# Kernel optimization log

Measured on AMD Instinct MI355X. Metric: run time of the kernel, lower is better.

Reference implementation:

```python
import jax, jax.numpy as jnp
import numpy as np
import math

B, S, I, C = 1, 512, 512, 256   # batch, n_seqs, n_res, c_in
H, D = 8, 32                    # num_heads, head_dim; total_dim = H*D = 256
TD = H * D


def setup_inputs() -> dict:
    key = jax.random.key(0)
    ks = jax.random.split(key, 12)
    w = lambda k, shape: (jax.random.normal(k, shape, dtype=jnp.float32) * 0.02)
    msa_representation = jax.random.normal(ks[0], (B, S, I, C), dtype=jnp.float32)
    msa_mask = (jax.random.uniform(ks[1], (B, S, I)) > 0.1).astype(jnp.float32)
    return {
        "msa_representation": msa_representation,
        "msa_mask": msa_mask,
        "ln_gamma": jnp.ones((C,), jnp.float32),
        "ln_beta": jnp.zeros((C,), jnp.float32),
        "Wq": w(ks[2], (C, TD)),
        "Wk": w(ks[3], (C, D)),
        "Wv": w(ks[4], (C, D)),
        "Wg": w(ks[5], (C, TD)),
        "bg": jnp.ones((TD,), jnp.float32),   # gate bias init = 1 (init_gate_linear)
        "Wo": w(ks[6], (TD, C)),
        "bo": jnp.zeros((C,), jnp.float32),
    }


def _layer_norm(x, gamma, beta, eps=1e-5):
    mu = jnp.mean(x, axis=-1, keepdims=True)
    var = jnp.mean(jnp.square(x - mu), axis=-1, keepdims=True)
    return (x - mu) * jax.lax.rsqrt(var + eps) * gamma + beta


def reference(msa_representation, msa_mask, ln_gamma, ln_beta,
              Wq, Wk, Wv, Wg, bg, Wo, bo):
    b, s, i, _ = msa_representation.shape
    x_ln = _layer_norm(msa_representation, ln_gamma, ln_beta)

    # Shared (head-less) K, V: [b, s, i, D]
    K = jnp.einsum('bsic,cd->bsid', x_ln, Wk)
    V = jnp.einsum('bsic,cd->bsid', x_ln, Wv)

    # Per-head query: [b, s, i, H, D]
    Q_si = jnp.einsum('bsic,ce->bsie', x_ln, Wq).reshape(b, s, i, H, D)

    # Masked mean-pool of the query over the sequence axis s -> [b, i, H, D]
    qm = msa_mask[..., None, None]                       # [b, s, i, 1, 1]
    Q = (Q_si * qm).sum(axis=1) / jnp.clip(qm.sum(axis=1), 1.0, None)

    # Sigmoid gate: [b, s, i, H, D]
    G = jax.nn.sigmoid(jnp.einsum('bsic,ce->bsie', x_ln, Wg) + bg).reshape(b, s, i, H, D)

    # Scores over the sequence axis t: [b, t, i, H]
    scores = jnp.einsum('bihc,btic->btih', Q, K) / math.sqrt(D)
    scores = scores + (1.0 - msa_mask[:, :, :, None]) * (-1e9)
    attention = jax.nn.softmax(scores, axis=1)

    # Weighted sum of shared V: [b, i, H, D], broadcast over s via gating
    weighted = jnp.einsum('btih,btic->bihc', attention, V)[:, None]  # [b,1,i,H,D]
    gated = (G * weighted).reshape(b, s, i, TD)
    output = jnp.einsum('bsie,ec->bsic', gated, Wo) + bo
    output = output * msa_mask[..., None]
    return output
```

## Files before the change

### kernel.cpp

```cpp
#include <hip/hip_runtime.h>

typedef __bf16 bf16_t;
typedef __bf16 bf16x4 __attribute__((ext_vector_type(4)));
typedef __bf16 bf16x8 __attribute__((ext_vector_type(8)));
typedef float f32x4 __attribute__((ext_vector_type(4)));

#define LXS 264

#define GLOAD_LDS16(gsrc, ldst) \
    __builtin_amdgcn_global_load_lds((__attribute__((address_space(1))) void*)(gsrc), \
                                     (__attribute__((address_space(3))) void*)(ldst), 16, 0, 0)

__global__ __launch_bounds__(256) void k_prep(
    const float* __restrict__ Wg, const float* __restrict__ Wo,
    const float* __restrict__ Wk, const float* __restrict__ Wv,
    bf16_t* __restrict__ WgP, bf16_t* __restrict__ WoP, bf16_t* __restrict__ WKVP)
{
    int id = blockIdx.x * 256 + threadIdx.x;
    if (id < 65536) {
        int j = id & 7, l = (id >> 3) & 63, kt = (id >> 9) & 7, nt = id >> 12;
        int k = kt * 32 + (l >> 4) * 8 + j;
        int n = nt * 16 + (l & 15);
        WgP[id] = (bf16_t)Wg[k * 256 + n];
    } else if (id < 131072) {
        int t = id - 65536;
        int j = t & 7, l = (t >> 3) & 63, kt = (t >> 9) & 7, nt = t >> 12;
        int k = kt * 32 + (l >> 4) * 8 + j;
        int n = nt * 16 + (l & 15);
        WoP[t] = (bf16_t)Wo[k * 256 + n];
    } else if (id < 147456) {
        int t = id - 131072;
        int j = t & 7, l = (t >> 3) & 63, kt = (t >> 9) & 7, nt = t >> 12;
        int k = kt * 32 + (l >> 4) * 8 + j;
        int n = nt * 16 + (l & 15);
        WKVP[t] = (bf16_t)(n < 32 ? Wk[k * 32 + n] : Wv[k * 32 + (n - 32)]);
    }
}

__global__ __launch_bounds__(256) void kA(
    const float* __restrict__ msa, const float* __restrict__ mask,
    const float* __restrict__ gamma, const float* __restrict__ beta,
    bf16_t* __restrict__ xln, bf16_t* __restrict__ kv, const bf16_t* __restrict__ WKVP,
    float* __restrict__ Qpart, float* __restrict__ Qcnt)
{
    __shared__ __align__(16) bf16_t lx[64 * LXS];
    __shared__ float pp[4][256];
    __shared__ float cw[4];
    int tid = threadIdx.x;
    int lane = tid & 63, w = tid >> 6;
    int l15 = lane & 15, l4 = lane >> 4;
    int i = blockIdx.x & 511;
    int schunk = blockIdx.x >> 9;
    int s0 = schunk * 64;

    float4 g4 = ((const float4*)gamma)[lane];
    float4 b4 = ((const float4*)beta)[lane];

    bf16x8 bfr[8];
    #pragma unroll
    for (int kt = 0; kt < 8; ++kt)
        bfr[kt] = *(const bf16x8*)(WKVP + ((w * 8 + kt) * 64 + lane) * 8);

    float p0 = 0, p1 = 0, p2 = 0, p3 = 0, pc = 0;
    for (int t = 0; t < 16; ++t) {
        int rl = w * 16 + t;
        size_t r = (size_t)(s0 + rl) * 512 + i;
        float4 x = ((const float4*)(msa + r * 256))[lane];
        float mv = mask[r];
        float s  = x.x + x.y + x.z + x.w;
        float ss = x.x*x.x + x.y*x.y + x.z*x.z + x.w*x.w;
        #pragma unroll
        for (int m = 32; m; m >>= 1) { s += __shfl_xor(s, m, 64); ss += __shfl_xor(ss, m, 64); }
        float mu = s * (1.0f / 256.0f);
        float var = ss * (1.0f / 256.0f) - mu * mu;
        float rs = rsqrtf(var + 1e-5f);
        float4 y;
        y.x = (x.x - mu) * rs * g4.x + b4.x;
        y.y = (x.y - mu) * rs * g4.y + b4.y;
        y.z = (x.z - mu) * rs * g4.z + b4.z;
        y.w = (x.w - mu) * rs * g4.w + b4.w;
        bf16x4 xv;
        xv[0] = (bf16_t)y.x; xv[1] = (bf16_t)y.y; xv[2] = (bf16_t)y.z; xv[3] = (bf16_t)y.w;
        *(bf16x4*)(xln + r * 256 + lane * 4) = xv;
        *(bf16x4*)(lx + rl * LXS + lane * 4) = xv;
        p0 += mv * y.x; p1 += mv * y.y; p2 += mv * y.z; p3 += mv * y.w;
        pc += mv;
    }
    *(float4*)&pp[w][lane * 4] = (float4){p0, p1, p2, p3};
    if (lane == 0) cw[w] = pc;
    __syncthreads();

    {
        float qs = pp[0][tid] + pp[1][tid] + pp[2][tid] + pp[3][tid];
        Qpart[((size_t)schunk * 512 + i) * 256 + tid] = qs;
        if (tid == 0) Qcnt[schunk * 512 + i] = cw[0] + cw[1] + cw[2] + cw[3];
    }

    f32x4 acc[4];
    #pragma unroll
    for (int rt = 0; rt < 4; ++rt) acc[rt] = (f32x4){0.f, 0.f, 0.f, 0.f};
    #pragma unroll
    for (int kt = 0; kt < 8; ++kt) {
        #pragma unroll
        for (int rt = 0; rt < 4; ++rt) {
            bf16x8 a = *(bf16x8*)(lx + (rt * 16 + l15) * LXS + kt * 32 + l4 * 8);
            acc[rt] = __builtin_amdgcn_mfma_f32_16x16x32_bf16(bfr[kt], a, acc[rt], 0, 0, 0);
        }
    }
    #pragma unroll
    for (int rt = 0; rt < 4; ++rt) {
        int row = rt * 16 + l15;
        size_t r = (size_t)(s0 + row) * 512 + i;
        bf16x4 kvv;
        #pragma unroll
        for (int j = 0; j < 4; ++j) kvv[j] = (bf16_t)acc[rt][j];
        *(bf16x4*)(kv + r * 64 + w * 16 + l4 * 4) = kvv;
    }
}

__global__ __launch_bounds__(256) void kB(
    const float* __restrict__ Qpart, const float* __restrict__ Qcnt,
    const float* __restrict__ Wq, float* __restrict__ Q)
{
    int i = blockIdx.x, tid = threadIdx.x;
    __shared__ float xs[256];
    float s = 0;
    #pragma unroll
    for (int ch = 0; ch < 8; ++ch) s += Qpart[((size_t)ch * 512 + i) * 256 + tid];
    xs[tid] = s;
    float cnt = 0;
    #pragma unroll
    for (int ch = 0; ch < 8; ++ch) cnt += Qcnt[ch * 512 + i];
    __syncthreads();
    float scale = 1.0f / (fmaxf(cnt, 1.0f) * 5.656854249492381f);
    float q = 0;
    for (int c = 0; c < 256; ++c) q += xs[c] * Wq[c * 256 + tid];
    Q[i * 256 + tid] = q * scale;
}

__global__ __launch_bounds__(256) void kC(
    const bf16_t* __restrict__ kv, const float* __restrict__ mask,
    const float* __restrict__ Q, float* __restrict__ wout)
{
    int i = blockIdx.x, tid = threadIdx.x;
    __shared__ __align__(16) bf16_t kbuf[512 * 32];
    __shared__ float sc[512 * 8];
    __shared__ float qq[256];
    __shared__ float mk[512];
    __shared__ float rcp[8];

    qq[tid] = Q[i * 256 + tid];
    mk[tid] = mask[tid * 512 + i];
    mk[tid + 256] = mask[(tid + 256) * 512 + i];

    for (int it = 0; it < 8; ++it) {
        int idx = it * 256 + tid; int t = idx >> 2; int q = idx & 3;
        ((uint4*)kbuf)[t * 4 + q] = ((const uint4*)kv)[((size_t)t * 512 + i) * 8 + q];
    }
    __syncthreads();

    for (int it = 0; it < 16; ++it) {
        int idx = it * 256 + tid; int t = idx >> 3; int h = idx & 7;
        float a = 0;
        #pragma unroll 8
        for (int d = 0; d < 32; ++d) a += qq[h * 32 + d] * (float)kbuf[t * 32 + d];
        sc[t * 8 + h] = a - (1.0f - mk[t]) * 1e9f;
    }
    __syncthreads();

    {
        int h = tid >> 5, l = tid & 31;
        float m = -1e30f;
        for (int k = 0; k < 16; ++k) m = fmaxf(m, sc[(l + 32 * k) * 8 + h]);
        #pragma unroll
        for (int off = 16; off; off >>= 1) m = fmaxf(m, __shfl_xor(m, off, 64));
        float s = 0;
        for (int k = 0; k < 16; ++k) {
            int idx = (l + 32 * k) * 8 + h;
            float p = __expf(sc[idx] - m);
            sc[idx] = p; s += p;
        }
        #pragma unroll
        for (int off = 16; off; off >>= 1) s += __shfl_xor(s, off, 64);
        if (l == 0) rcp[h] = 1.0f / s;
    }
    for (int it = 0; it < 8; ++it) {
        int idx = it * 256 + tid; int t = idx >> 2; int q = idx & 3;
        ((uint4*)kbuf)[t * 4 + q] = ((const uint4*)kv)[((size_t)t * 512 + i) * 8 + 4 + q];
    }
    __syncthreads();

    {
        int h = tid >> 5, d = tid & 31;
        float acc = 0;
        for (int t = 0; t < 512; ++t) acc += sc[t * 8 + h] * (float)kbuf[t * 32 + d];
        wout[i * 256 + tid] = acc * rcp[h];
    }
}

__global__ __launch_bounds__(256, 3) void kD(
    const bf16_t* __restrict__ xln, const bf16_t* __restrict__ WgP, const bf16_t* __restrict__ WoP,
    const float* __restrict__ bg, const float* __restrict__ bo,
    const float* __restrict__ weighted, const float* __restrict__ mask, float* __restrict__ out)
{
    __shared__ __align__(16) bf16_t lx[64 * 256];
    int tid = threadIdx.x;
    int lane = tid & 63, q = tid >> 6;
    int l15 = lane & 15, l4 = lane >> 4;
    int swb = l15 & 7;
    int rowbase = blockIdx.x * 64;

    const bf16_t* sB = xln + (size_t)rowbase * 256;
    #pragma unroll
    for (int c = 0; c < 8; ++c) {
        int idx = (c * 256 + tid) * 16;
        int row_ = idx >> 9;
        int g_ = (idx >> 4) & 31;
        GLOAD_LDS16(sB + row_ * 256 + (g_ ^ (row_ & 7)) * 8, lx + c * 2048 + q * 512);
    }
    __syncthreads();

#define LOADW(DST, WP, KT) \
    _Pragma("unroll") \
    for (int ctl = 0; ctl < 4; ++ctl) \
        DST[ctl] = *(const bf16x8*)((WP) + ((((q * 4 + ctl) * 8 + (KT)) * 64 + lane) * 8));

#define GSTEP(BW, KT) \
    { bf16x8 a2[4]; \
      _Pragma("unroll") \
      for (int rt = 0; rt < 4; ++rt) \
          a2[rt] = *(bf16x8*)(lx + (rt * 16 + l15) * 256 + (((KT) * 4 + l4) ^ swb) * 8); \
      _Pragma("unroll") \
      for (int ctl = 0; ctl < 4; ++ctl) \
          _Pragma("unroll") \
          for (int rt = 0; rt < 4; ++rt) \
              acc[rt][ctl] = __builtin_amdgcn_mfma_f32_16x16x32_bf16(BW[ctl], a2[rt], acc[rt][ctl], 0, 0, 0); }

    f32x4 acc[4][4];
    bf16x8 bA[4], bB[4];

    #pragma unroll
    for (int rt = 0; rt < 4; ++rt)
        #pragma unroll
        for (int ctl = 0; ctl < 4; ++ctl) acc[rt][ctl] = (f32x4){0.f, 0.f, 0.f, 0.f};
    LOADW(bA, WgP, 0)
    LOADW(bB, WgP, 1)
    GSTEP(bA, 0) LOADW(bA, WgP, 2)
    GSTEP(bB, 1) LOADW(bB, WgP, 3)
    GSTEP(bA, 2) LOADW(bA, WgP, 4)
    GSTEP(bB, 3) LOADW(bB, WgP, 5)
    GSTEP(bA, 4) LOADW(bA, WgP, 6)
    GSTEP(bB, 5) LOADW(bB, WgP, 7)
    GSTEP(bA, 6)
    GSTEP(bB, 7)
    __syncthreads();

    #pragma unroll
    for (int ctl = 0; ctl < 4; ++ctl) {
        int c4 = (q * 4 + ctl) * 16 + l4 * 4;
        float4 bg4 = *(const float4*)(bg + c4);
        int g0 = c4 >> 3, c7 = c4 & 7;
        #pragma unroll
        for (int rt = 0; rt < 4; ++rt) {
            int row = rt * 16 + l15;
            int i2 = (rowbase + row) & 511;
            float4 w4 = *(const float4*)(weighted + i2 * 256 + c4);
            f32x4 t4 = acc[rt][ctl];
            bf16x4 gv;
            gv[0] = (bf16_t)(w4.x / (1.0f + __expf(-(t4[0] + bg4.x))));
            gv[1] = (bf16_t)(w4.y / (1.0f + __expf(-(t4[1] + bg4.y))));
            gv[2] = (bf16_t)(w4.z / (1.0f + __expf(-(t4[2] + bg4.z))));
            gv[3] = (bf16_t)(w4.w / (1.0f + __expf(-(t4[3] + bg4.w))));
            *(bf16x4*)(lx + row * 256 + ((g0 ^ (row & 7)) << 3) + c7) = gv;
        }
    }
    __syncthreads();

    #pragma unroll
    for (int rt = 0; rt < 4; ++rt)
        #pragma unroll
        for (int ctl = 0; ctl < 4; ++ctl) acc[rt][ctl] = (f32x4){0.f, 0.f, 0.f, 0.f};
    LOADW(bA, WoP, 0)
    LOADW(bB, WoP, 1)
    GSTEP(bA, 0) LOADW(bA, WoP, 2)
    GSTEP(bB, 1) LOADW(bB, WoP, 3)
    GSTEP(bA, 2) LOADW(bA, WoP, 4)
    GSTEP(bB, 3) LOADW(bB, WoP, 5)
    GSTEP(bA, 4) LOADW(bA, WoP, 6)
    GSTEP(bB, 5) LOADW(bB, WoP, 7)
    GSTEP(bA, 6)
    GSTEP(bB, 7)

    #pragma unroll
    for (int ctl = 0; ctl < 4; ++ctl) {
        int c4 = (q * 4 + ctl) * 16 + l4 * 4;
        float4 bo4 = *(const float4*)(bo + c4);
        #pragma unroll
        for (int rt = 0; rt < 4; ++rt) {
            int r = rowbase + rt * 16 + l15;
            float mv = mask[r];
            f32x4 o;
            o[0] = (acc[rt][ctl][0] + bo4.x) * mv;
            o[1] = (acc[rt][ctl][1] + bo4.y) * mv;
            o[2] = (acc[rt][ctl][2] + bo4.z) * mv;
            o[3] = (acc[rt][ctl][3] + bo4.w) * mv;
            __builtin_nontemporal_store(o, (f32x4*)(out + (size_t)r * 256 + c4));
        }
    }
#undef LOADW
#undef GSTEP
}

extern "C" void kernel_launch(void* const* d_in, const int* in_sizes, int n_in,
                              void* d_out, int out_size, void* d_ws, size_t ws_size,
                              hipStream_t stream) {
    const float* msa   = (const float*)d_in[0];
    const float* mask  = (const float*)d_in[1];
    const float* gamma = (const float*)d_in[2];
    const float* beta  = (const float*)d_in[3];
    const float* Wq    = (const float*)d_in[4];
    const float* Wk    = (const float*)d_in[5];
    const float* Wv    = (const float*)d_in[6];
    const float* Wg    = (const float*)d_in[7];
    const float* bg    = (const float*)d_in[8];
    const float* Wo    = (const float*)d_in[9];
    const float* bo    = (const float*)d_in[10];
    float* out = (float*)d_out;

    char* ws = (char*)d_ws;
    bf16_t* xln   = (bf16_t*)(ws);
    bf16_t* kv    = (bf16_t*)(ws + 134217728);
    float*  Qp    = (float*)(ws + 167772160);
    float*  wgt   = (float*)(ws + 168296448);
    bf16_t* WgP   = (bf16_t*)(ws + 168820736);
    bf16_t* WoP   = (bf16_t*)(ws + 168951808);
    bf16_t* WKVP  = (bf16_t*)(ws + 169082880);
    float*  Qpart = (float*)(ws + 169115648);
    float*  Qcnt  = (float*)(ws + 173309952);

    k_prep<<<576, 256, 0, stream>>>(Wg, Wo, Wk, Wv, WgP, WoP, WKVP);
    kA<<<4096, 256, 0, stream>>>(msa, mask, gamma, beta, xln, kv, WKVP, Qpart, Qcnt);
    kB<<<512, 256, 0, stream>>>(Qpart, Qcnt, Wq, Qp);
    kC<<<512, 256, 0, stream>>>(kv, mask, Qp, wgt);
    kD<<<4096, 256, 0, stream>>>(xln, WgP, WoP, bg, bo, wgt, mask, out);
}
```

Measured before the change: 282.6 us.

## Split attention over sequence chunks with flash-style merge and enlarge gate/output tiles

```diff
diff --git a/kernel.cpp b/kernel.cpp
--- a/kernel.cpp
+++ b/kernel.cpp
@@ -138,28 +138,31 @@
     Q[i * 256 + tid] = q * scale;
 }
 
-__global__ __launch_bounds__(256) void kC(
-    const bf16_t* __restrict__ kv, const float* __restrict__ mask,
-    const float* __restrict__ Q, float* __restrict__ wout)
-{
-    int i = blockIdx.x, tid = threadIdx.x;
-    __shared__ __align__(16) bf16_t kbuf[512 * 32];
-    __shared__ float sc[512 * 8];
+__global__ __launch_bounds__(256) void kC1(
+    const bf16_t* __restrict__ kv, const float* __restrict__ mask, const float* __restrict__ Q,
+    float* __restrict__ Wp, float* __restrict__ Mp, float* __restrict__ Lp)
+{
+    int i = blockIdx.x & 511, ch = blockIdx.x >> 9;
+    int t0 = ch * 128;
+    int tid = threadIdx.x;
+    __shared__ __align__(16) bf16_t kbuf[128 * 32];
+    __shared__ float sc[128 * 8];
     __shared__ float qq[256];
-    __shared__ float mk[512];
-    __shared__ float rcp[8];
+    __shared__ float mk[128];
+    __shared__ float mred[8], lred[8];
 
     qq[tid] = Q[i * 256 + tid];
-    mk[tid] = mask[tid * 512 + i];
-    mk[tid + 256] = mask[(tid + 256) * 512 + i];
-
-    for (int it = 0; it < 8; ++it) {
+    if (tid < 128) mk[tid] = mask[(size_t)(t0 + tid) * 512 + i];
+
+    #pragma unroll
+    for (int it = 0; it < 2; ++it) {
         int idx = it * 256 + tid; int t = idx >> 2; int q = idx & 3;
-        ((uint4*)kbuf)[t * 4 + q] = ((const uint4*)kv)[((size_t)t * 512 + i) * 8 + q];
-    }
-    __syncthreads();
-
-    for (int it = 0; it < 16; ++it) {
+        ((uint4*)kbuf)[t * 4 + q] = ((const uint4*)kv)[((size_t)(t0 + t) * 512 + i) * 8 + q];
+    }
+    __syncthreads();
+
+    #pragma unroll
+    for (int it = 0; it < 4; ++it) {
         int idx = it * 256 + tid; int t = idx >> 3; int h = idx & 7;
         float a = 0;
         #pragma unroll 8
@@ -168,55 +171,87 @@
     }
     __syncthreads();
 
+    #pragma unroll
+    for (int it = 0; it < 2; ++it) {
+        int idx = it * 256 + tid; int t = idx >> 2; int q = idx & 3;
+        ((uint4*)kbuf)[t * 4 + q] = ((const uint4*)kv)[((size_t)(t0 + t) * 512 + i) * 8 + 4 + q];
+    }
     {
         int h = tid >> 5, l = tid & 31;
-        float m = -1e30f;
-        for (int k = 0; k < 16; ++k) m = fmaxf(m, sc[(l + 32 * k) * 8 + h]);
-        #pragma unroll
-        for (int off = 16; off; off >>= 1) m = fmaxf(m, __shfl_xor(m, off, 64));
+        float m = -3e38f;
+        #pragma unroll
+        for (int k = 0; k < 4; ++k) m = fmaxf(m, sc[(l + 32 * k) * 8 + h]);
+        #pragma unroll
+        for (int off = 16; off; off >>= 1) m = fmaxf(m, __shfl_xor(m, off, 32));
         float s = 0;
-        for (int k = 0; k < 16; ++k) {
+        #pragma unroll
+        for (int k = 0; k < 4; ++k) {
             int idx = (l + 32 * k) * 8 + h;
             float p = __expf(sc[idx] - m);
             sc[idx] = p; s += p;
         }
         #pragma unroll
-        for (int off = 16; off; off >>= 1) s += __shfl_xor(s, off, 64);
-        if (l == 0) rcp[h] = 1.0f / s;
-    }
-    for (int it = 0; it < 8; ++it) {
-        int idx = it * 256 + tid; int t = idx >> 2; int q = idx & 3;
-        ((uint4*)kbuf)[t * 4 + q] = ((const uint4*)kv)[((size_t)t * 512 + i) * 8 + 4 + q];
+        for (int off = 16; off; off >>= 1) s += __shfl_xor(s, off, 32);
+        if (l == 0) { mred[h] = m; lred[h] = s; }
     }
     __syncthreads();
 
     {
         int h = tid >> 5, d = tid & 31;
-        float acc = 0;
-        for (int t = 0; t < 512; ++t) acc += sc[t * 8 + h] * (float)kbuf[t * 32 + d];
-        wout[i * 256 + tid] = acc * rcp[h];
-    }
-}
-
-__global__ __launch_bounds__(256, 3) void kD(
+        float a = 0;
+        for (int t = 0; t < 128; ++t) a += sc[t * 8 + h] * (float)kbuf[t * 32 + d];
+        Wp[((size_t)ch * 512 + i) * 256 + tid] = a;
+    }
+    if (tid < 8) {
+        Mp[((size_t)ch * 512 + i) * 8 + tid] = mred[tid];
+        Lp[((size_t)ch * 512 + i) * 8 + tid] = lred[tid];
+    }
+}
+
+__global__ __launch_bounds__(256) void kC2(
+    const float* __restrict__ Wp, const float* __restrict__ Mp, const float* __restrict__ Lp,
+    float* __restrict__ wgt)
+{
+    int i = blockIdx.x, tid = threadIdx.x;
+    int h = tid >> 5;
+    float m[4], l[4];
+    #pragma unroll
+    for (int ch = 0; ch < 4; ++ch) {
+        m[ch] = Mp[((size_t)ch * 512 + i) * 8 + h];
+        l[ch] = Lp[((size_t)ch * 512 + i) * 8 + h];
+    }
+    float M = fmaxf(fmaxf(m[0], m[1]), fmaxf(m[2], m[3]));
+    float den = 0, num = 0;
+    #pragma unroll
+    for (int ch = 0; ch < 4; ++ch) {
+        float e = __expf(m[ch] - M);
+        den += l[ch] * e;
+        num += Wp[((size_t)ch * 512 + i) * 256 + tid] * e;
+    }
+    wgt[i * 256 + tid] = num / den;
+}
+
+__global__ __launch_bounds__(512, 4) void kD(
     const bf16_t* __restrict__ xln, const bf16_t* __restrict__ WgP, const bf16_t* __restrict__ WoP,
     const float* __restrict__ bg, const float* __restrict__ bo,
     const float* __restrict__ weighted, const float* __restrict__ mask, float* __restrict__ out)
 {
-    __shared__ __align__(16) bf16_t lx[64 * 256];
+    __shared__ __align__(16) bf16_t lx[128 * 256];
     int tid = threadIdx.x;
-    int lane = tid & 63, q = tid >> 6;
+    int lane = tid & 63, w = tid >> 6;
+    int h = w >> 2, q = w & 3;
     int l15 = lane & 15, l4 = lane >> 4;
     int swb = l15 & 7;
-    int rowbase = blockIdx.x * 64;
+    int rowbase = blockIdx.x * 128;
+    int rbase = h * 64;
 
     const bf16_t* sB = xln + (size_t)rowbase * 256;
     #pragma unroll
     for (int c = 0; c < 8; ++c) {
-        int idx = (c * 256 + tid) * 16;
+        int idx = (c * 512 + tid) * 16;
         int row_ = idx >> 9;
         int g_ = (idx >> 4) & 31;
-        GLOAD_LDS16(sB + row_ * 256 + (g_ ^ (row_ & 7)) * 8, lx + c * 2048 + q * 512);
+        GLOAD_LDS16(sB + row_ * 256 + (g_ ^ (row_ & 7)) * 8, lx + c * 4096 + w * 512);
     }
     __syncthreads();
 
@@ -229,7 +264,7 @@
     { bf16x8 a2[4]; \
       _Pragma("unroll") \
       for (int rt = 0; rt < 4; ++rt) \
-          a2[rt] = *(bf16x8*)(lx + (rt * 16 + l15) * 256 + (((KT) * 4 + l4) ^ swb) * 8); \
+          a2[rt] = *(bf16x8*)(lx + (rbase + rt * 16 + l15) * 256 + (((KT) * 4 + l4) ^ swb) * 8); \
       _Pragma("unroll") \
       for (int ctl = 0; ctl < 4; ++ctl) \
           _Pragma("unroll") \
@@ -262,7 +297,7 @@
         int g0 = c4 >> 3, c7 = c4 & 7;
         #pragma unroll
         for (int rt = 0; rt < 4; ++rt) {
-            int row = rt * 16 + l15;
+            int row = rbase + rt * 16 + l15;
             int i2 = (rowbase + row) & 511;
             float4 w4 = *(const float4*)(weighted + i2 * 256 + c4);
             f32x4 t4 = acc[rt][ctl];
@@ -297,14 +332,14 @@
         float4 bo4 = *(const float4*)(bo + c4);
         #pragma unroll
         for (int rt = 0; rt < 4; ++rt) {
-            int r = rowbase + rt * 16 + l15;
+            int r = rowbase + rbase + rt * 16 + l15;
             float mv = mask[r];
             f32x4 o;
             o[0] = (acc[rt][ctl][0] + bo4.x) * mv;
             o[1] = (acc[rt][ctl][1] + bo4.y) * mv;
             o[2] = (acc[rt][ctl][2] + bo4.z) * mv;
             o[3] = (acc[rt][ctl][3] + bo4.w) * mv;
-            __builtin_nontemporal_store(o, (f32x4*)(out + (size_t)r * 256 + c4));
+            *(f32x4*)(out + (size_t)r * 256 + c4) = o;
         }
     }
 #undef LOADW
@@ -337,10 +372,14 @@
     bf16_t* WKVP  = (bf16_t*)(ws + 169082880);
     float*  Qpart = (float*)(ws + 169115648);
     float*  Qcnt  = (float*)(ws + 173309952);
+    float*  Wp    = (float*)(ws + 169115648);
+    float*  Mp    = (float*)(ws + 173326336);
+    float*  Lp    = (float*)(ws + 173391872);
 
     k_prep<<<576, 256, 0, stream>>>(Wg, Wo, Wk, Wv, WgP, WoP, WKVP);
     kA<<<4096, 256, 0, stream>>>(msa, mask, gamma, beta, xln, kv, WKVP, Qpart, Qcnt);
     kB<<<512, 256, 0, stream>>>(Qpart, Qcnt, Wq, Qp);
-    kC<<<512, 256, 0, stream>>>(kv, mask, Qp, wgt);
-    kD<<<4096, 256, 0, stream>>>(xln, WgP, WoP, bg, bo, wgt, mask, out);
-}
+    kC1<<<2048, 256, 0, stream>>>(kv, mask, Qp, Wp, Mp, Lp);
+    kC2<<<512, 256, 0, stream>>>(Wp, Mp, Lp, wgt);
+    kD<<<2048, 512, 0, stream>>>(xln, WgP, WoP, bg, bo, wgt, mask, out);
+}
```

After: 338.3 us. 19.7% more time.

## Keep xln tile in registers for gate GEMM and drop LDS staging barrier

Applied to the files above, without the earlier changes.

```diff
diff --git a/kernel.cpp b/kernel.cpp
--- a/kernel.cpp
+++ b/kernel.cpp
@@ -6,10 +6,6 @@
 typedef float f32x4 __attribute__((ext_vector_type(4)));
 
 #define LXS 264
-
-#define GLOAD_LDS16(gsrc, ldst) \
-    __builtin_amdgcn_global_load_lds((__attribute__((address_space(1))) void*)(gsrc), \
-                                     (__attribute__((address_space(3))) void*)(ldst), 16, 0, 0)
 
 __global__ __launch_bounds__(256) void k_prep(
     const float* __restrict__ Wg, const float* __restrict__ Wo,
@@ -198,25 +194,72 @@
     }
 }
 
-__global__ __launch_bounds__(256, 3) void kD(
+__global__ __launch_bounds__(256, 2) void kD(
     const bf16_t* __restrict__ xln, const bf16_t* __restrict__ WgP, const bf16_t* __restrict__ WoP,
     const float* __restrict__ bg, const float* __restrict__ bo,
     const float* __restrict__ weighted, const float* __restrict__ mask, float* __restrict__ out)
 {
-    __shared__ __align__(16) bf16_t lx[64 * 256];
+    __shared__ __align__(16) bf16_t gl[64 * 256];
     int tid = threadIdx.x;
     int lane = tid & 63, q = tid >> 6;
     int l15 = lane & 15, l4 = lane >> 4;
     int swb = l15 & 7;
     int rowbase = blockIdx.x * 64;
 
-    const bf16_t* sB = xln + (size_t)rowbase * 256;
-    #pragma unroll
-    for (int c = 0; c < 8; ++c) {
-        int idx = (c * 256 + tid) * 16;
-        int row_ = idx >> 9;
-        int g_ = (idx >> 4) & 31;
-        GLOAD_LDS16(sB + row_ * 256 + (g_ ^ (row_ & 7)) * 8, lx + c * 2048 + q * 512);
+    bf16x8 xf[4][8];
+    #pragma unroll
+    for (int kt = 0; kt < 8; ++kt)
+        #pragma unroll
+        for (int rt = 0; rt < 4; ++rt)
+            xf[rt][kt] = *(const bf16x8*)(xln + (size_t)(rowbase + rt * 16 + l15) * 256 + kt * 32 + l4 * 8);
+
+#define LOADW2(DST, WP, CT0, KT) \
+    { DST[0] = *(const bf16x8*)((WP) + ((((CT0) * 8 + (KT)) * 64 + lane) * 8)); \
+      DST[1] = *(const bf16x8*)((WP) + ((((CT0 + 1) * 8 + (KT)) * 64 + lane) * 8)); }
+
+#define GSTEP1(BW, KT, AH) \
+    _Pragma("unroll") \
+    for (int c2 = 0; c2 < 2; ++c2) \
+        _Pragma("unroll") \
+        for (int rt = 0; rt < 4; ++rt) \
+            AH[rt][c2] = __builtin_amdgcn_mfma_f32_16x16x32_bf16(BW[c2], xf[rt][KT], AH[rt][c2], 0, 0, 0);
+
+    #pragma unroll
+    for (int halfc = 0; halfc < 2; ++halfc) {
+        int ct0 = q * 4 + halfc * 2;
+        f32x4 ah[4][2];
+        #pragma unroll
+        for (int rt = 0; rt < 4; ++rt) { ah[rt][0] = (f32x4){0.f,0.f,0.f,0.f}; ah[rt][1] = (f32x4){0.f,0.f,0.f,0.f}; }
+        bf16x8 bA[2], bB[2];
+        LOADW2(bA, WgP, ct0, 0)
+        LOADW2(bB, WgP, ct0, 1)
+        GSTEP1(bA, 0, ah) LOADW2(bA, WgP, ct0, 2)
+        GSTEP1(bB, 1, ah) LOADW2(bB, WgP, ct0, 3)
+        GSTEP1(bA, 2, ah) LOADW2(bA, WgP, ct0, 4)
+        GSTEP1(bB, 3, ah) LOADW2(bB, WgP, ct0, 5)
+        GSTEP1(bA, 4, ah) LOADW2(bA, WgP, ct0, 6)
+        GSTEP1(bB, 5, ah) LOADW2(bB, WgP, ct0, 7)
+        GSTEP1(bA, 6, ah)
+        GSTEP1(bB, 7, ah)
+        #pragma unroll
+        for (int c2 = 0; c2 < 2; ++c2) {
+            int c4 = (ct0 + c2) * 16 + l4 * 4;
+            float4 bg4 = *(const float4*)(bg + c4);
+            int g0 = c4 >> 3, c7 = c4 & 7;
+            #pragma unroll
+            for (int rt = 0; rt < 4; ++rt) {
+                int row = rt * 16 + l15;
+                int i2 = (rowbase + row) & 511;
+                float4 w4 = *(const float4*)(weighted + i2 * 256 + c4);
+                f32x4 t4 = ah[rt][c2];
+                bf16x4 gv;
+                gv[0] = (bf16_t)(w4.x / (1.0f + __expf(-(t4[0] + bg4.x))));
+                gv[1] = (bf16_t)(w4.y / (1.0f + __expf(-(t4[1] + bg4.y))));
+                gv[2] = (bf16_t)(w4.z / (1.0f + __expf(-(t4[2] + bg4.z))));
+                gv[3] = (bf16_t)(w4.w / (1.0f + __expf(-(t4[3] + bg4.w))));
+                *(bf16x4*)(gl + row * 256 + ((g0 ^ (row & 7)) << 3) + c7) = gv;
+            }
+        }
     }
     __syncthreads();
 
@@ -229,7 +272,7 @@
     { bf16x8 a2[4]; \
       _Pragma("unroll") \
       for (int rt = 0; rt < 4; ++rt) \
-          a2[rt] = *(bf16x8*)(lx + (rt * 16 + l15) * 256 + (((KT) * 4 + l4) ^ swb) * 8); \
+          a2[rt] = *(bf16x8*)(gl + (rt * 16 + l15) * 256 + (((KT) * 4 + l4) ^ swb) * 8); \
       _Pragma("unroll") \
       for (int ctl = 0; ctl < 4; ++ctl) \
           _Pragma("unroll") \
@@ -238,44 +281,6 @@
 
     f32x4 acc[4][4];
     bf16x8 bA[4], bB[4];
-
-    #pragma unroll
-    for (int rt = 0; rt < 4; ++rt)
-        #pragma unroll
-        for (int ctl = 0; ctl < 4; ++ctl) acc[rt][ctl] = (f32x4){0.f, 0.f, 0.f, 0.f};
-    LOADW(bA, WgP, 0)
-    LOADW(bB, WgP, 1)
-    GSTEP(bA, 0) LOADW(bA, WgP, 2)
-    GSTEP(bB, 1) LOADW(bB, WgP, 3)
-    GSTEP(bA, 2) LOADW(bA, WgP, 4)
-    GSTEP(bB, 3) LOADW(bB, WgP, 5)
-    GSTEP(bA, 4) LOADW(bA, WgP, 6)
-    GSTEP(bB, 5) LOADW(bB, WgP, 7)
-    GSTEP(bA, 6)
-    GSTEP(bB, 7)
-    __syncthreads();
-
-    #pragma unroll
-    for (int ctl = 0; ctl < 4; ++ctl) {
-        int c4 = (q * 4 + ctl) * 16 + l4 * 4;
-        float4 bg4 = *(const float4*)(bg + c4);
-        int g0 = c4 >> 3, c7 = c4 & 7;
-        #pragma unroll
-        for (int rt = 0; rt < 4; ++rt) {
-            int row = rt * 16 + l15;
-            int i2 = (rowbase + row) & 511;
-            float4 w4 = *(const float4*)(weighted + i2 * 256 + c4);
-            f32x4 t4 = acc[rt][ctl];
-            bf16x4 gv;
-            gv[0] = (bf16_t)(w4.x / (1.0f + __expf(-(t4[0] + bg4.x))));
-            gv[1] = (bf16_t)(w4.y / (1.0f + __expf(-(t4[1] + bg4.y))));
-            gv[2] = (bf16_t)(w4.z / (1.0f + __expf(-(t4[2] + bg4.z))));
-            gv[3] = (bf16_t)(w4.w / (1.0f + __expf(-(t4[3] + bg4.w))));
-            *(bf16x4*)(lx + row * 256 + ((g0 ^ (row & 7)) << 3) + c7) = gv;
-        }
-    }
-    __syncthreads();
-
     #pragma unroll
     for (int rt = 0; rt < 4; ++rt)
         #pragma unroll
@@ -308,7 +313,9 @@
         }
     }
 #undef LOADW
+#undef LOADW2
 #undef GSTEP
+#undef GSTEP1
 }
 
 extern "C" void kernel_launch(void* const* d_in, const int* in_sizes, int n_in,
```

Measured after the change: 321.9 us. 13.9% more time.
